# Performance work log

Hardware: AMD Instinct MI355X
Metric: run time of the kernel (lower is better)

## Reference

```python
import jax, jax.numpy as jnp
import numpy as np

N, M, K, C = 2048, 2048, 32, 256
AW, NE, H, S = 32, 128, 8, 32
LMAX = 2
HID = min(128, AW // 2)          # 16, hidden width of radial MLPs
EC = AW + NE + C                 # 416, edge feature dim
M0 = 2 * AW * (LMAX + 1)         # 192, q/k degree-dot feature dim
SLICES = [(0, 1), (1, 4), (4, 9)]  # m-slices for l = 0, 1, 2


def _ln(x, g, b, eps=1e-5):
    mu = jnp.mean(x, -1, keepdims=True)
    var = jnp.mean(jnp.square(x - mu), -1, keepdims=True)
    return (x - mu) * jax.lax.rsqrt(var + eps) * g + b


def _radial(x, w1, b1, g1, be1, w2, b2, g2, be2, w3, b3):
    # EquiformerV2-style RadialFunction: Linear->LN->SiLU x2 -> Linear
    h = jax.nn.silu(_ln(x @ w1.T + b1, g1, be1))
    h = jax.nn.silu(_ln(h @ w2.T + b2, g2, be2))
    return h @ w3.T + b3


def _so3_linear(x, W, b):
    # per-degree channel mixing; bias only on l=0. x: [..., 9, Cin], W: [3, Cout, Cin]
    outs = []
    for l, (s, e) in enumerate(SLICES):
        o = jnp.einsum('...mc,dc->...md', x[..., s:e, :], W[l])
        if l == 0:
            o = o + b
        outs.append(o)
    return jnp.concatenate(outs, axis=-2)


def _sph_all(vec):
    # real spherical harmonics l=0..2 of normalized vec, integral normalization
    v = vec / (jnp.linalg.norm(vec, axis=-1, keepdims=True) + 1e-12)
    x, y, z = v[..., 0], v[..., 1], v[..., 2]
    y0 = jnp.full(x.shape, 0.28209479177387814)
    c1 = 0.4886025119029199
    c2a, c2b, c2c = 1.0925484305920792, 0.31539156525252005, 0.5462742152960396
    return jnp.stack([y0, c1 * y, c1 * z, c1 * x,
                      c2a * x * y, c2a * y * z, c2b * (3.0 * z * z - 1.0),
                      c2a * x * z, c2c * (x * x - y * y)], axis=-1)


def _smooth_leaky(x, a=0.2):
    return 0.5 * (1 + a) * x + 0.5 * (1 - a) * x * (2.0 * jax.nn.sigmoid(x) - 1.0)


def _forward(node_pos, node_irreps_input, edge_dis, edge_vec, attn_weight,
             cluster_irreps_input, tgt_emb, W_dot, b_dot,
             rm0_w1, rm0_b1, rm0_g1, rm0_be1, rm0_w2, rm0_b2, rm0_g2, rm0_be2, rm0_w3, rm0_b3,
             fc_m0_w, fc_m0_b, an_g, an_b, alpha_dot,
             rv_w1, rv_b1, rv_g1, rv_be1, rv_w2, rv_b2, rv_g2, rv_be2, rv_w3, rv_b3,
             wz, bz, atomic_numbers, attn_mask, f_sparse_idx_expnode):
    n, k = attn_weight.shape[0], attn_weight.shape[1]
    aw = jnp.where(attn_mask, 0.0, attn_weight)                 # mask padded neighbors
    tgt = tgt_emb[atomic_numbers]                               # [N,NE]
    idx = f_sparse_idx_expnode                                  # [N,K] cluster gather index
    cl_scal = cluster_irreps_input[:, 0, :][idx]                # [N,K,C] scalar (l=0) part
    x_edge = jnp.concatenate(
        [aw, jnp.broadcast_to(tgt[:, None, :], (n, k, tgt.shape[-1])), cl_scal], -1)

    # dot_alpha attention logits: per-degree <feat, Y_l(r_ij)> for query and gathered key
    q = _so3_linear(node_irreps_input, W_dot, b_dot)            # [N,9,AW]
    key = _so3_linear(cluster_irreps_input, W_dot, b_dot)[idx]  # [N,K,9,AW]
    sh = _sph_all(edge_vec)                                     # [N,K,9]
    dots = [jnp.einsum('nmc,nkm->nkc', q[:, s:e, :], sh[..., s:e]) for s, e in SLICES]
    dots += [jnp.einsum('nkmc,nkm->nkc', key[:, :, s:e, :], sh[..., s:e]) for s, e in SLICES]
    m0 = jnp.concatenate(dots, -1)                              # [N,K,M0]

    ew = _radial(x_edge, rm0_w1, rm0_b1, rm0_g1, rm0_be1, rm0_w2, rm0_b2, rm0_g2, rm0_be2, rm0_w3, rm0_b3)
    af = ((m0 * ew) @ fc_m0_w.T + fc_m0_b).reshape(n, k, H, S)
    af = _smooth_leaky(_ln(af, an_g, an_b))
    logits = jnp.einsum('nkhs,hs->nkh', af, alpha_dot)
    logits = jnp.where(attn_mask, -1e9, logits)
    alpha = jax.nn.softmax(logits, axis=1)                      # [N,K,H]

    # zero-order value path: radial edge weight modulates gathered equivariant values
    vw = _radial(x_edge, rv_w1, rv_b1, rv_g1, rv_be1, rv_w2, rv_b2, rv_g2, rv_be2, rv_w3, rv_b3)
    v = (cluster_irreps_input[idx] * vw[:, :, None, :]).reshape(n, k, 9, H, C // H)
    out = jnp.einsum('nkh,nkmhc->nmhc', alpha, v).reshape(n, 9, C)
    return _so3_linear(out, wz, bz)                             # [N,9,C]


def setup_inputs() -> dict:
    ks = iter(jax.random.split(jax.random.key(0), 64))
    nrm = lambda shape, s=1.0: jax.random.normal(next(ks), shape, jnp.float32) * s
    inp = {}
    inp['node_pos'] = nrm((N, 3))
    inp['node_irreps_input'] = nrm((N, 9, C))
    inp['edge_dis'] = jax.random.uniform(next(ks), (N, K), jnp.float32) * 5.0
    inp['edge_vec'] = nrm((N, K, 3))
    inp['attn_weight'] = nrm((N, K, AW))
    inp['atomic_numbers'] = jax.random.randint(next(ks), (N,), 0, 256)
    inp['attn_mask'] = jax.random.bernoulli(next(ks), 0.1, (N, K, 1))
    inp['f_sparse_idx_expnode'] = jax.random.randint(next(ks), (N, K), 0, M)
    inp['cluster_irreps_input'] = nrm((M, 9, C))
    inp['tgt_emb'] = jax.random.uniform(next(ks), (256, NE), jnp.float32, -0.001, 0.001)
    inp['W_dot'] = nrm((3, AW, C), C ** -0.5)
    inp['b_dot'] = jnp.zeros((AW,), jnp.float32)

    def rad_params(pfx, out_dim):
        d = {}
        d[pfx + '_w1'] = nrm((HID, EC), EC ** -0.5); d[pfx + '_b1'] = jnp.zeros((HID,), jnp.float32)
        d[pfx + '_g1'] = jnp.ones((HID,), jnp.float32); d[pfx + '_be1'] = jnp.zeros((HID,), jnp.float32)
        d[pfx + '_w2'] = nrm((HID, HID), HID ** -0.5); d[pfx + '_b2'] = jnp.zeros((HID,), jnp.float32)
        d[pfx + '_g2'] = jnp.ones((HID,), jnp.float32); d[pfx + '_be2'] = jnp.zeros((HID,), jnp.float32)
        d[pfx + '_w3'] = nrm((out_dim, HID), HID ** -0.5); d[pfx + '_b3'] = jnp.zeros((out_dim,), jnp.float32)
        return d

    inp.update(rad_params('rm0', M0))
    inp['fc_m0_w'] = nrm((H * S, M0), M0 ** -0.5)
    inp['fc_m0_b'] = jnp.zeros((H * S,), jnp.float32)
    inp['an_g'] = jnp.ones((S,), jnp.float32)
    inp['an_b'] = jnp.zeros((S,), jnp.float32)
    std = S ** -0.5
    inp['alpha_dot'] = jax.random.uniform(next(ks), (H, S), jnp.float32, -std, std)
    inp.update(rad_params('rv', C))
    inp['wz'] = nrm((3, C, C), C ** -0.5)
    inp['bz'] = jnp.zeros((C,), jnp.float32)
    return inp


def reference(node_pos, node_irreps_input, edge_dis, edge_vec, attn_weight, atomic_numbers,
              attn_mask, f_sparse_idx_expnode, cluster_irreps_input, tgt_emb, W_dot, b_dot,
              rm0_w1, rm0_b1, rm0_g1, rm0_be1, rm0_w2, rm0_b2, rm0_g2, rm0_be2, rm0_w3, rm0_b3,
              fc_m0_w, fc_m0_b, an_g, an_b, alpha_dot,
              rv_w1, rv_b1, rv_g1, rv_be1, rv_w2, rv_b2, rv_g2, rv_be2, rv_w3, rv_b3,
              wz, bz):
    return _forward(node_pos, node_irreps_input, edge_dis, edge_vec, attn_weight,
                    cluster_irreps_input, tgt_emb, W_dot, b_dot,
                    rm0_w1, rm0_b1, rm0_g1, rm0_be1, rm0_w2, rm0_b2, rm0_g2, rm0_be2, rm0_w3, rm0_b3,
                    fc_m0_w, fc_m0_b, an_g, an_b, alpha_dot,
                    rv_w1, rv_b1, rv_g1, rv_be1, rv_w2, rv_b2, rv_g2, rv_be2, rv_w3, rv_b3,
                    wz, bz, atomic_numbers, attn_mask, f_sparse_idx_expnode)
```

## Files before the change

kernel.cpp:

```cpp
#include <hip/hip_runtime.h>
#include <math.h>

#define NNODE 2048
#define MCLUS 2048
#define KNBR  32
#define CDIM  256
#define HHEAD 8

typedef __attribute__((ext_vector_type(8))) short bf16x8;
typedef __attribute__((ext_vector_type(4))) float f32x4;

__device__ __forceinline__ float sigf(float x) { return 1.0f / (1.0f + __expf(-x)); }

__device__ __forceinline__ unsigned short f2bf(float f) {
    unsigned x = __float_as_uint(f);
    unsigned r = ((x >> 16) & 1u) + 0x7FFFu;
    return (unsigned short)((x + r) >> 16);
}
__device__ __forceinline__ float bf2f(unsigned short u) {
    return __uint_as_float(((unsigned)u) << 16);
}

__device__ __forceinline__ bool edge_masked(const void* mp, int mode, int e) {
    if (mode & 2) return ((const float*)mp)[e] != 0.0f;
    if (mode & 1) return ((const unsigned char*)mp)[e] != 0;
    return ((const int*)mp)[e] != 0;
}

__global__ __launch_bounds__(256) void kprep(
    const unsigned int* __restrict__ mw, int* __restrict__ flag,
    const float* __restrict__ clus, const float* __restrict__ fcw,
    const float* __restrict__ wz,
    unsigned short* __restrict__ clh, unsigned short* __restrict__ fcwh,
    unsigned short* __restrict__ wzh,
    const float* __restrict__ tgt_emb,
    const float* __restrict__ rm0_w1, const float* __restrict__ rv_w1,
    float* __restrict__ TA, float* __restrict__ CA,
    const float* __restrict__ nodei, const float* __restrict__ W_dot,
    const float* __restrict__ b_dot,
    float* __restrict__ q_ws, unsigned short* __restrict__ keyh)
{
    __shared__ __align__(16) unsigned short Xb[32][264];
    __shared__ __align__(16) unsigned short Wb[32][264];
    __shared__ int rx[32], rmm[32];
    int b = blockIdx.x, t = threadIdx.x;

    if (b < 1152) {
        int l, vr0, nm, moff;
        if (b < 128)      { l = 0; vr0 = b * 32;         nm = 1; moff = 0; }
        else if (b < 512) { l = 1; vr0 = (b - 128) * 32; nm = 3; moff = 1; }
        else              { l = 2; vr0 = (b - 512) * 32; nm = 5; moff = 4; }
        if (t < 32) {
            int vr = vr0 + t;
            rx[t] = vr / nm;
            rmm[t] = moff + vr % nm;
        }
        __syncthreads();
        for (int e = t; e < 32 * 256; e += 256) {
            int r = e >> 8, c = e & 255;
            int x = rx[r], m = rmm[r];
            const float* src = (x < NNODE) ? (nodei + ((size_t)x * 9 + m) * 256)
                                           : (clus + ((size_t)(x - NNODE) * 9 + m) * 256);
            Xb[r][c] = f2bf(src[c]);
            Wb[r][c] = f2bf(W_dot[((size_t)l * 32 + r) * 256 + c]);
        }
        __syncthreads();

        int wid = t >> 6, lane = t & 63;
        int lrow = lane & 15, kgrp = lane >> 4;
        int mt = wid >> 1, nt = wid & 1;
        f32x4 acc = (f32x4){0.f, 0.f, 0.f, 0.f};
#pragma unroll
        for (int kk = 0; kk < 8; ++kk) {
            bf16x8 a8 = *(const bf16x8*)&Xb[mt * 16 + lrow][kk * 32 + kgrp * 8];
            bf16x8 b8 = *(const bf16x8*)&Wb[nt * 16 + lrow][kk * 32 + kgrp * 8];
            acc = __builtin_amdgcn_mfma_f32_16x16x32_bf16(a8, b8, acc, 0, 0, 0);
        }
        int dcol = nt * 16 + lrow;
        float bias = (l == 0) ? b_dot[dcol] : 0.0f;
#pragma unroll
        for (int r = 0; r < 4; ++r) {
            int row = mt * 16 + kgrp * 4 + r;
            int x = rx[row], m = rmm[row];
            float val = acc[r] + bias;
            if (x < NNODE) q_ws[((size_t)x * 9 + m) * 32 + dcol] = val;
            else           keyh[((size_t)(x - NNODE) * 9 + m) * 32 + dcol] = f2bf(val);
        }
    } else if (b < 4160) {
        int bb = b - 1152;
        if (bb < MCLUS) {
            size_t base = (size_t)bb * 2304;
#pragma unroll
            for (int r = 0; r < 9; ++r) {
                int o = r * 256 + t;
                clh[base + o] = f2bf(clus[base + o]);
            }
        } else if (bb < MCLUS + 192) {
            int off = (bb - MCLUS) * 256 + t;
            fcwh[off] = f2bf(fcw[off]);
        } else {
            int off = (bb - MCLUS - 192) * 256 + t;
            wzh[off] = f2bf(wz[off]);
        }
    } else if (b < 4448) {
        int bb = b - 4160;
        int slot = t & 31, j = slot & 15, mlp = slot >> 4;
        const float* w1 = mlp ? rv_w1 : rm0_w1;
        if (bb < 32) {
            int a = bb * 8 + (t >> 5);
            const float* x = tgt_emb + (size_t)a * 128;
            const float* w = w1 + j * 416 + 32;
            float acc = 0.0f;
            for (int i = 0; i < 128; i += 4)
                acc = fmaf(x[i], w[i], fmaf(x[i+1], w[i+1], fmaf(x[i+2], w[i+2], fmaf(x[i+3], w[i+3], acc))));
            TA[a * 32 + slot] = acc;
        } else {
            int m = (bb - 32) * 8 + (t >> 5);
            const float* x = clus + (size_t)m * 2304;
            const float* w = w1 + j * 416 + 160;
            float acc = 0.0f;
            for (int i = 0; i < 256; i += 4)
                acc = fmaf(x[i], w[i], fmaf(x[i+1], w[i+1], fmaf(x[i+2], w[i+2], fmaf(x[i+3], w[i+3], acc))));
            CA[m * 32 + slot] = acc;
        }
    } else {
        int i = (b - 4448) * 256 + t;
        unsigned int w = mw[i];
        int vb = (w != 0u && w != 1u && w != 0x3F800000u) ? 1 : 0;
        int vf = (w == 0x3F800000u) ? 1 : 0;
        unsigned long long bal_b = __ballot(vb);
        unsigned long long bal_f = __ballot(vf);
        if ((t & 63) == 0) {
            if (bal_b) atomicOr(flag, 1);
            if (bal_f) atomicOr(flag, 2);
        }
    }
}

__device__ __forceinline__ float lnsilu16(float x, float g, float b) {
    float s = x;
#pragma unroll
    for (int m = 1; m < 16; m <<= 1) s += __shfl_xor(s, m, 16);
    float mu = s * 0.0625f;
    float d = x - mu;
    float s2 = d * d;
#pragma unroll
    for (int m = 1; m < 16; m <<= 1) s2 += __shfl_xor(s2, m, 16);
    float y = d * rsqrtf(s2 * 0.0625f + 1e-5f) * g + b;
    return y * sigf(y);
}

__global__ __launch_bounds__(256, 2) void k2abc(
    const float* __restrict__ attn_weight, const void* __restrict__ mask,
    const int* __restrict__ mflag,
    const int* __restrict__ f_idx, const float* __restrict__ edge_vec,
    const int* __restrict__ atom_num, const unsigned short* __restrict__ clh,
    const float* __restrict__ q_ws, const unsigned short* __restrict__ keyh,
    const float* __restrict__ TA, const float* __restrict__ CA,
    const float* __restrict__ rm0_w1, const float* __restrict__ rm0_b1,
    const float* __restrict__ rm0_g1, const float* __restrict__ rm0_be1,
    const float* __restrict__ rm0_w2, const float* __restrict__ rm0_b2,
    const float* __restrict__ rm0_g2, const float* __restrict__ rm0_be2,
    const float* __restrict__ rm0_w3, const float* __restrict__ rm0_b3,
    const unsigned short* __restrict__ fcwh, const float* __restrict__ fcb,
    const float* __restrict__ an_g, const float* __restrict__ an_b,
    const float* __restrict__ alpha_dot,
    const float* __restrict__ rv_w1, const float* __restrict__ rv_b1,
    const float* __restrict__ rv_g1, const float* __restrict__ rv_be1,
    const float* __restrict__ rv_w2, const float* __restrict__ rv_b2,
    const float* __restrict__ rv_g2, const float* __restrict__ rv_be2,
    const float* __restrict__ rv_w3, const float* __restrict__ rv_b3,
    float* __restrict__ outpre)
{
    __shared__ float qn[288];
    __shared__ float Ts[32];
    __shared__ float shS[32][9];
    __shared__ __align__(16) unsigned char poolS[32 * 200 * 2];
    float (*awS)[32] = (float(*)[32])poolS;
    float (*caS)[32] = (float(*)[32])(poolS + 4096);
    unsigned short (*mwbS)[200] = (unsigned short(*)[200])poolS;
    __shared__ unsigned short KDSh[32][96];
    __shared__ float h2mS[32][17];
    __shared__ float h2vS[32][17];
    __shared__ float lgS[32][8];
    __shared__ float alS[256];
    __shared__ float mxS[8], invS[8];
    __shared__ int idxk[32], maskk[32];

    int n = blockIdx.x, t = threadIdx.x;
    int mode = mflag[0];

    for (int i = t; i < 288; i += 256) qn[i] = q_ws[(size_t)n * 288 + i];
    if (t < 32) {
        int an = atom_num[n];
        Ts[t] = TA[an * 32 + t];
        int e = n * KNBR + t;
        idxk[t] = f_idx[e];
        maskk[t] = edge_masked(mask, mode, e) ? 1 : 0;
        float vx = edge_vec[(size_t)e * 3 + 0];
        float vy = edge_vec[(size_t)e * 3 + 1];
        float vz = edge_vec[(size_t)e * 3 + 2];
        float inv = 1.0f / (sqrtf(vx * vx + vy * vy + vz * vz) + 1e-12f);
        float x = vx * inv, y = vy * inv, z = vz * inv;
        shS[t][0] = 0.28209479177387814f;
        shS[t][1] = 0.4886025119029199f * y;
        shS[t][2] = 0.4886025119029199f * z;
        shS[t][3] = 0.4886025119029199f * x;
        shS[t][4] = 1.0925484305920792f * x * y;
        shS[t][5] = 1.0925484305920792f * y * z;
        shS[t][6] = 0.31539156525252005f * (3.0f * z * z - 1.0f);
        shS[t][7] = 1.0925484305920792f * x * z;
        shS[t][8] = 0.5462742152960396f * (x * x - y * y);
    }
    __syncthreads();
    for (int e2 = t; e2 < 1024; e2 += 256) {
        int ek = e2 >> 5, i = e2 & 31;
        awS[ek][i] = maskk[ek] ? 0.0f : attn_weight[((size_t)(n * KNBR + ek)) * 32 + i];
        caS[ek][i] = CA[(size_t)idxk[ek] * 32 + i];
    }
    for (int i = t; i < 32 * 96; i += 256) {
        int e = i / 96, j = i - e * 96;
        int p = j >> 5, c = j & 31;
        const unsigned short* kr = keyh + (size_t)idxk[e] * 288;
        float v;
        if (p == 0)      v = bf2f(kr[c]) * shS[e][0];
        else if (p == 1) v = bf2f(kr[32 + c]) * shS[e][1] + bf2f(kr[64 + c]) * shS[e][2]
                           + bf2f(kr[96 + c]) * shS[e][3];
        else             v = bf2f(kr[128 + c]) * shS[e][4] + bf2f(kr[160 + c]) * shS[e][5]
                           + bf2f(kr[192 + c]) * shS[e][6] + bf2f(kr[224 + c]) * shS[e][7]
                           + bf2f(kr[256 + c]) * shS[e][8];
        KDSh[e][j] = f2bf(v);
    }
    __syncthreads();

    {
        int g = t >> 4, j = t & 15;
        for (int ee = 0; ee < 2; ++ee) {
            int e = g + ee * 16;
            float accm = rm0_b1[j] + Ts[j] + caS[e][j];
            float accv = rv_b1[j] + Ts[16 + j] + caS[e][16 + j];
            const float* w1m = rm0_w1 + j * 416;
            const float* w1v = rv_w1 + j * 416;
#pragma unroll
            for (int i = 0; i < 32; i += 4) {
                float a0 = awS[e][i], a1 = awS[e][i + 1], a2 = awS[e][i + 2], a3 = awS[e][i + 3];
                accm = fmaf(a0, w1m[i], fmaf(a1, w1m[i+1], fmaf(a2, w1m[i+2], fmaf(a3, w1m[i+3], accm))));
                accv = fmaf(a0, w1v[i], fmaf(a1, w1v[i+1], fmaf(a2, w1v[i+2], fmaf(a3, w1v[i+3], accv))));
            }
            float hm = lnsilu16(accm, rm0_g1[j], rm0_be1[j]);
            float hv = lnsilu16(accv, rv_g1[j], rv_be1[j]);
            float am2 = rm0_b2[j], av2 = rv_b2[j];
#pragma unroll
            for (int i = 0; i < 16; ++i) {
                am2 = fmaf(__shfl(hm, i, 16), rm0_w2[j * 16 + i], am2);
                av2 = fmaf(__shfl(hv, i, 16), rv_w2[j * 16 + i], av2);
            }
            float h2m = lnsilu16(am2, rm0_g2[j], rm0_be2[j]);
            float h2v = lnsilu16(av2, rv_g2[j], rv_be2[j]);
            h2vS[e][j] = h2v;
            h2mS[e][j] = h2m;
        }
    }
    __syncthreads();

#pragma unroll
    for (int bb = 0; bb < 6; ++bb) {
#pragma unroll
        for (int r2 = 0; r2 < 4; ++r2) {
            int oi = r2 * 256 + t;
            int e = oi >> 5, c = oi & 31;
            int d = bb * 32 + c;
            const float4* w3 = (const float4*)(rm0_w3 + d * 16);
            float ew = rm0_b3[d];
#pragma unroll
            for (int i4 = 0; i4 < 4; ++i4) {
                float4 w = w3[i4];
                ew = fmaf(h2mS[e][i4 * 4 + 0], w.x, fmaf(h2mS[e][i4 * 4 + 1], w.y,
                     fmaf(h2mS[e][i4 * 4 + 2], w.z, fmaf(h2mS[e][i4 * 4 + 3], w.w, ew))));
            }
            float m0v;
            if (bb == 0)      m0v = qn[c] * shS[e][0];
            else if (bb == 1) m0v = qn[32 + c] * shS[e][1] + qn[64 + c] * shS[e][2]
                                  + qn[96 + c] * shS[e][3];
            else if (bb == 2) m0v = qn[128 + c] * shS[e][4] + qn[160 + c] * shS[e][5]
                                  + qn[192 + c] * shS[e][6] + qn[224 + c] * shS[e][7]
                                  + qn[256 + c] * shS[e][8];
            else              m0v = bf2f(KDSh[e][(bb - 3) * 32 + c]);
            mwbS[e][d] = f2bf(ew * m0v);
        }
    }
    __syncthreads();

    {
        int wid = t >> 6, lane = t & 63;
        int lrow = lane & 15, kgrp = lane >> 4;
        f32x4 acc[4][2];
#pragma unroll
        for (int i = 0; i < 4; ++i)
#pragma unroll
            for (int m = 0; m < 2; ++m) acc[i][m] = (f32x4){0.f, 0.f, 0.f, 0.f};

#pragma unroll
        for (int ntl = 0; ntl < 4; ++ntl) {
            int col = wid * 64 + ntl * 16 + lrow;
            const bf16x8* brow = (const bf16x8*)(fcwh + (size_t)col * 192);
            bf16x8 bf[6];
#pragma unroll
            for (int kk = 0; kk < 6; ++kk) bf[kk] = brow[kk * 4 + kgrp];
#pragma unroll
            for (int kk = 0; kk < 6; ++kk) {
#pragma unroll
                for (int m = 0; m < 2; ++m) {
                    bf16x8 a8 = *(const bf16x8*)&mwbS[m * 16 + lrow][kk * 32 + kgrp * 8];
                    acc[ntl][m] = __builtin_amdgcn_mfma_f32_16x16x32_bf16(a8, bf[kk], acc[ntl][m], 0, 0, 0);
                }
            }
        }
#pragma unroll
        for (int ntl = 0; ntl < 4; ++ntl) {
            float fb = fcb[wid * 64 + ntl * 16 + lrow];
#pragma unroll
            for (int m = 0; m < 2; ++m)
#pragma unroll
                for (int r = 0; r < 4; ++r) acc[ntl][m][r] += fb;
        }
        float ang0 = an_g[lrow], ang1 = an_g[16 + lrow];
        float anb0 = an_b[lrow], anb1 = an_b[16 + lrow];
#pragma unroll
        for (int hh = 0; hh < 2; ++hh) {
            int h = wid * 2 + hh;
            float ad0 = alpha_dot[h * 32 + lrow], ad1 = alpha_dot[h * 32 + 16 + lrow];
#pragma unroll
            for (int m = 0; m < 2; ++m) {
#pragma unroll
                for (int r = 0; r < 4; ++r) {
                    float a = acc[2 * hh][m][r], b = acc[2 * hh + 1][m][r];
                    float su = a + b;
#pragma unroll
                    for (int mm = 1; mm < 16; mm <<= 1) su += __shfl_xor(su, mm, 16);
                    float mu = su * (1.0f / 32.0f);
                    float da = a - mu, db = b - mu;
                    float v2 = da * da + db * db;
#pragma unroll
                    for (int mm = 1; mm < 16; mm <<= 1) v2 += __shfl_xor(v2, mm, 16);
                    float rs = rsqrtf(v2 * (1.0f / 32.0f) + 1e-5f);
                    float y0 = da * rs * ang0 + anb0;
                    float y1 = db * rs * ang1 + anb1;
                    float sl0 = 0.6f * y0 + 0.4f * y0 * (2.0f * sigf(y0) - 1.0f);
                    float sl1 = 0.6f * y1 + 0.4f * y1 * (2.0f * sigf(y1) - 1.0f);
                    float lg = sl0 * ad0 + sl1 * ad1;
#pragma unroll
                    for (int mm = 1; mm < 16; mm <<= 1) lg += __shfl_xor(lg, mm, 16);
                    if (lrow == 0) {
                        int e = m * 16 + kgrp * 4 + r;
                        lgS[e][h] = maskk[e] ? -1e9f : lg;
                    }
                }
            }
        }
    }
    __syncthreads();

    if (t < 8) {
        float mx = -1e30f;
#pragma unroll
        for (int k = 0; k < 32; ++k) mx = fmaxf(mx, lgS[k][t]);
        float sum = 0.0f;
#pragma unroll
        for (int k = 0; k < 32; ++k) sum += __expf(lgS[k][t] - mx);
        mxS[t] = mx;
        invS[t] = 1.0f / sum;
    }
    __syncthreads();
    {
        int k = t >> 3, h = t & 7;
        alS[t] = __expf(lgS[k][h] - mxS[h]) * invS[h];
    }
    __syncthreads();

    {
        int c = t, h = c >> 5;
        float w3r[16];
        const float4* w3p = (const float4*)(rv_w3 + c * 16);
#pragma unroll
        for (int i4 = 0; i4 < 4; ++i4) {
            float4 w = w3p[i4];
            w3r[i4 * 4 + 0] = w.x; w3r[i4 * 4 + 1] = w.y;
            w3r[i4 * 4 + 2] = w.z; w3r[i4 * 4 + 3] = w.w;
        }
        float b3c = rv_b3[c];
        float acc[9];
#pragma unroll
        for (int m = 0; m < 9; ++m) acc[m] = 0.0f;
        for (int k = 0; k < 32; ++k) {
            float vw = b3c;
#pragma unroll
            for (int i = 0; i < 16; ++i) vw = fmaf(h2vS[k][i], w3r[i], vw);
            float av = alS[k * 8 + h] * vw;
            const unsigned short* crow = clh + (size_t)idxk[k] * 2304 + c;
#pragma unroll
            for (int m = 0; m < 9; ++m) acc[m] = fmaf(av, bf2f(crow[m * 256]), acc[m]);
        }
#pragma unroll
        for (int m = 0; m < 9; ++m) outpre[((size_t)n * 9 + m) * 256 + c] = acc[m];
    }
}

__global__ __launch_bounds__(256) void k5_final(
    const unsigned short* __restrict__ wzh, const float* __restrict__ bz,
    float* __restrict__ io)
{
    __shared__ __align__(16) unsigned short Xb[32][264];
    __shared__ int rr[32];
    int b = blockIdx.x, t = threadIdx.x;
    int l, vr0, nm, moff;
    if (b < 64)       { l = 0; vr0 = b * 32;         nm = 1; moff = 0; }
    else if (b < 256) { l = 1; vr0 = (b - 64) * 32;  nm = 3; moff = 1; }
    else              { l = 2; vr0 = (b - 256) * 32; nm = 5; moff = 4; }
    if (t < 32) {
        int vr = vr0 + t;
        int n = vr / nm, m = moff + vr % nm;
        rr[t] = n * 9 + m;
    }
    __syncthreads();
    for (int e = t; e < 32 * 256; e += 256) {
        int r = e >> 8, c = e & 255;
        Xb[r][c] = f2bf(io[(size_t)rr[r] * 256 + c]);
    }
    __syncthreads();

    int wid = t >> 6, lane = t & 63;
    int lrow = lane & 15, kgrp = lane >> 4;
    f32x4 acc[2][4];
#pragma unroll
    for (int mt = 0; mt < 2; ++mt)
#pragma unroll
        for (int ntl = 0; ntl < 4; ++ntl) acc[mt][ntl] = (f32x4){0.f, 0.f, 0.f, 0.f};

#pragma unroll
    for (int ntl = 0; ntl < 4; ++ntl) {
        int dcol = wid * 64 + ntl * 16 + lrow;
        const bf16x8* brow = (const bf16x8*)(wzh + ((size_t)l * 256 + dcol) * 256);
#pragma unroll
        for (int kk = 0; kk < 8; ++kk) {
            bf16x8 b8 = brow[kk * 4 + kgrp];
#pragma unroll
            for (int mt = 0; mt < 2; ++mt) {
                bf16x8 a8 = *(const bf16x8*)&Xb[mt * 16 + lrow][kk * 32 + kgrp * 8];
                acc[mt][ntl] = __builtin_amdgcn_mfma_f32_16x16x32_bf16(a8, b8, acc[mt][ntl], 0, 0, 0);
            }
        }
    }
#pragma unroll
    for (int ntl = 0; ntl < 4; ++ntl) {
        int dcol = wid * 64 + ntl * 16 + lrow;
        float bias = (l == 0) ? bz[dcol] : 0.0f;
#pragma unroll
        for (int mt = 0; mt < 2; ++mt) {
#pragma unroll
            for (int r = 0; r < 4; ++r) {
                int row = mt * 16 + kgrp * 4 + r;
                io[(size_t)rr[row] * 256 + dcol] = acc[mt][ntl][r] + bias;
            }
        }
    }
}

extern "C" void kernel_launch(void* const* d_in, const int* in_sizes, int n_in,
                              void* d_out, int out_size, void* d_ws, size_t ws_size,
                              hipStream_t stream)
{
    (void)in_sizes; (void)n_in; (void)out_size; (void)ws_size;

    const float* node_irreps = (const float*)d_in[1];
    const float* edge_vec    = (const float*)d_in[3];
    const float* attn_weight = (const float*)d_in[4];
    const int*   atom_num    = (const int*)d_in[5];
    const void*  attn_mask   = d_in[6];
    const int*   f_idx       = (const int*)d_in[7];
    const float* clus        = (const float*)d_in[8];
    const float* tgt_emb     = (const float*)d_in[9];
    const float* W_dot       = (const float*)d_in[10];
    const float* b_dot       = (const float*)d_in[11];
    const float* rm0_w1 = (const float*)d_in[12];
    const float* rm0_b1 = (const float*)d_in[13];
    const float* rm0_g1 = (const float*)d_in[14];
    const float* rm0_be1 = (const float*)d_in[15];
    const float* rm0_w2 = (const float*)d_in[16];
    const float* rm0_b2 = (const float*)d_in[17];
    const float* rm0_g2 = (const float*)d_in[18];
    const float* rm0_be2 = (const float*)d_in[19];
    const float* rm0_w3 = (const float*)d_in[20];
    const float* rm0_b3 = (const float*)d_in[21];
    const float* fcw = (const float*)d_in[22];
    const float* fcb = (const float*)d_in[23];
    const float* an_g = (const float*)d_in[24];
    const float* an_b = (const float*)d_in[25];
    const float* alpha_dot = (const float*)d_in[26];
    const float* rv_w1 = (const float*)d_in[27];
    const float* rv_b1 = (const float*)d_in[28];
    const float* rv_g1 = (const float*)d_in[29];
    const float* rv_be1 = (const float*)d_in[30];
    const float* rv_w2 = (const float*)d_in[31];
    const float* rv_b2 = (const float*)d_in[32];
    const float* rv_g2 = (const float*)d_in[33];
    const float* rv_be2 = (const float*)d_in[34];
    const float* rv_w3 = (const float*)d_in[35];
    const float* rv_b3 = (const float*)d_in[36];
    const float* wz = (const float*)d_in[37];
    const float* bz = (const float*)d_in[38];

    float* ws = (float*)d_ws;
    int* flag = (int*)d_ws;
    float* q_ws = ws + 16;
    unsigned short* keyh = (unsigned short*)(q_ws + (size_t)NNODE * 288);
    float* TA_ws = (float*)(keyh + (size_t)MCLUS * 288);
    float* CA_ws = TA_ws + 256 * 32;
    unsigned short* clh = (unsigned short*)(CA_ws + (size_t)MCLUS * 32);
    unsigned short* fcwh = (unsigned short*)(clh + (size_t)MCLUS * 2304);
    unsigned short* wzh = fcwh + 256 * 192;
    float* outpre = (float*)d_out;

    hipMemsetAsync(flag, 0, sizeof(int), stream);
    kprep<<<4512, 256, 0, stream>>>(
        (const unsigned int*)attn_mask, flag,
        clus, fcw, wz, clh, fcwh, wzh,
        tgt_emb, rm0_w1, rv_w1, TA_ws, CA_ws,
        node_irreps, W_dot, b_dot, q_ws, keyh);
    k2abc<<<NNODE, 256, 0, stream>>>(
        attn_weight, attn_mask, flag, f_idx, edge_vec, atom_num, clh,
        q_ws, keyh, TA_ws, CA_ws,
        rm0_w1, rm0_b1, rm0_g1, rm0_be1, rm0_w2, rm0_b2, rm0_g2, rm0_be2, rm0_w3, rm0_b3,
        fcwh, fcb, an_g, an_b, alpha_dot,
        rv_w1, rv_b1, rv_g1, rv_be1, rv_w2, rv_b2, rv_g2, rv_be2, rv_w3, rv_b3,
        outpre);
    k5_final<<<576, 256, 0, stream>>>(wzh, bz, outpre);
}
```

Measured before the change: 198.7 us.

## Fuse final SO3 linear into attention kernel and skip masked edges

Folds the separate final per-degree linear (k5_final) into the end of the per-node attention kernel. Each block now writes its 9x256 pre-activation to shared memory as bf16, zero-pads it to 16 rows, and runs MFMA against all three degree weight matrices, writing only the rows that belong to each degree. This removes a launch and the global write/read round trip of the intermediate, but spends about 3x the MFMA work per node on padded or unused rows. It also skips masked edges in the value accumulation loop and overlays several shared arrays to limit LDS growth.

```diff
diff --git a/kernel.cpp b/kernel.cpp
--- a/kernel.cpp
+++ b/kernel.cpp
@@ -150,7 +150,7 @@
     return y * sigf(y);
 }
 
-__global__ __launch_bounds__(256, 2) void k2abc(
+__global__ __launch_bounds__(256, 2) void k2full(
     const float* __restrict__ attn_weight, const void* __restrict__ mask,
     const int* __restrict__ mflag,
     const int* __restrict__ f_idx, const float* __restrict__ edge_vec,
@@ -170,7 +170,8 @@
     const float* __restrict__ rv_w2, const float* __restrict__ rv_b2,
     const float* __restrict__ rv_g2, const float* __restrict__ rv_be2,
     const float* __restrict__ rv_w3, const float* __restrict__ rv_b3,
-    float* __restrict__ outpre)
+    const unsigned short* __restrict__ wzh, const float* __restrict__ bz,
+    float* __restrict__ outfin)
 {
     __shared__ float qn[288];
     __shared__ float Ts[32];
@@ -179,12 +180,15 @@
     float (*awS)[32] = (float(*)[32])poolS;
     float (*caS)[32] = (float(*)[32])(poolS + 4096);
     unsigned short (*mwbS)[200] = (unsigned short(*)[200])poolS;
-    __shared__ unsigned short KDSh[32][96];
+    unsigned short (*XbD)[264] = (unsigned short(*)[264])poolS;
+    __shared__ __align__(16) unsigned char pool2[6144];
+    unsigned short (*KDSh)[96] = (unsigned short(*)[96])pool2;
+    float (*lgS)[8] = (float(*)[8])pool2;
+    float* alS = (float*)(pool2 + 1024);
+    float* mxS = (float*)(pool2 + 2048);
+    float* invS = (float*)(pool2 + 2080);
     __shared__ float h2mS[32][17];
     __shared__ float h2vS[32][17];
-    __shared__ float lgS[32][8];
-    __shared__ float alS[256];
-    __shared__ float mxS[8], invS[8];
     __shared__ int idxk[32], maskk[32];
 
     int n = blockIdx.x, t = threadIdx.x;
@@ -393,6 +397,7 @@
 #pragma unroll
         for (int m = 0; m < 9; ++m) acc[m] = 0.0f;
         for (int k = 0; k < 32; ++k) {
+            if (maskk[k]) continue;
             float vw = b3c;
 #pragma unroll
             for (int i = 0; i < 16; ++i) vw = fmaf(h2vS[k][i], w3r[i], vw);
@@ -401,66 +406,43 @@
 #pragma unroll
             for (int m = 0; m < 9; ++m) acc[m] = fmaf(av, bf2f(crow[m * 256]), acc[m]);
         }
-#pragma unroll
-        for (int m = 0; m < 9; ++m) outpre[((size_t)n * 9 + m) * 256 + c] = acc[m];
-    }
-}
-
-__global__ __launch_bounds__(256) void k5_final(
-    const unsigned short* __restrict__ wzh, const float* __restrict__ bz,
-    float* __restrict__ io)
-{
-    __shared__ __align__(16) unsigned short Xb[32][264];
-    __shared__ int rr[32];
-    int b = blockIdx.x, t = threadIdx.x;
-    int l, vr0, nm, moff;
-    if (b < 64)       { l = 0; vr0 = b * 32;         nm = 1; moff = 0; }
-    else if (b < 256) { l = 1; vr0 = (b - 64) * 32;  nm = 3; moff = 1; }
-    else              { l = 2; vr0 = (b - 256) * 32; nm = 5; moff = 4; }
-    if (t < 32) {
-        int vr = vr0 + t;
-        int n = vr / nm, m = moff + vr % nm;
-        rr[t] = n * 9 + m;
-    }
-    __syncthreads();
-    for (int e = t; e < 32 * 256; e += 256) {
-        int r = e >> 8, c = e & 255;
-        Xb[r][c] = f2bf(io[(size_t)rr[r] * 256 + c]);
-    }
-    __syncthreads();
-
-    int wid = t >> 6, lane = t & 63;
-    int lrow = lane & 15, kgrp = lane >> 4;
-    f32x4 acc[2][4];
-#pragma unroll
-    for (int mt = 0; mt < 2; ++mt)
-#pragma unroll
-        for (int ntl = 0; ntl < 4; ++ntl) acc[mt][ntl] = (f32x4){0.f, 0.f, 0.f, 0.f};
-
-#pragma unroll
-    for (int ntl = 0; ntl < 4; ++ntl) {
-        int dcol = wid * 64 + ntl * 16 + lrow;
-        const bf16x8* brow = (const bf16x8*)(wzh + ((size_t)l * 256 + dcol) * 256);
-#pragma unroll
-        for (int kk = 0; kk < 8; ++kk) {
-            bf16x8 b8 = brow[kk * 4 + kgrp];
-#pragma unroll
-            for (int mt = 0; mt < 2; ++mt) {
-                bf16x8 a8 = *(const bf16x8*)&Xb[mt * 16 + lrow][kk * 32 + kgrp * 8];
-                acc[mt][ntl] = __builtin_amdgcn_mfma_f32_16x16x32_bf16(a8, b8, acc[mt][ntl], 0, 0, 0);
-            }
-        }
-    }
-#pragma unroll
-    for (int ntl = 0; ntl < 4; ++ntl) {
-        int dcol = wid * 64 + ntl * 16 + lrow;
-        float bias = (l == 0) ? bz[dcol] : 0.0f;
-#pragma unroll
-        for (int mt = 0; mt < 2; ++mt) {
-#pragma unroll
-            for (int r = 0; r < 4; ++r) {
-                int row = mt * 16 + kgrp * 4 + r;
-                io[(size_t)rr[row] * 256 + dcol] = acc[mt][ntl][r] + bias;
+        __syncthreads();
+#pragma unroll
+        for (int m = 0; m < 9; ++m) XbD[m][c] = f2bf(acc[m]);
+        for (int i = t; i < 7 * 256; i += 256) XbD[9 + (i >> 8)][i & 255] = 0;
+    }
+    __syncthreads();
+
+    {
+        int wid = t >> 6, lane = t & 63;
+        int lrow = lane & 15, kgrp = lane >> 4;
+        bf16x8 a8v[8];
+#pragma unroll
+        for (int kk = 0; kk < 8; ++kk)
+            a8v[kk] = *(const bf16x8*)&XbD[lrow][kk * 32 + kgrp * 8];
+#pragma unroll
+        for (int l = 0; l < 3; ++l) {
+#pragma unroll
+            for (int ntl = 0; ntl < 4; ++ntl) {
+                int dcol = wid * 64 + ntl * 16 + lrow;
+                const bf16x8* brow = (const bf16x8*)(wzh + ((size_t)l * 256 + dcol) * 256);
+                f32x4 acc = (f32x4){0.f, 0.f, 0.f, 0.f};
+#pragma unroll
+                for (int kk = 0; kk < 8; ++kk) {
+                    bf16x8 b8 = brow[kk * 4 + kgrp];
+                    acc = __builtin_amdgcn_mfma_f32_16x16x32_bf16(a8v[kk], b8, acc, 0, 0, 0);
+                }
+#pragma unroll
+                for (int r = 0; r < 4; ++r) {
+                    int m = kgrp * 4 + r;
+                    bool valid = (l == 0) ? (m == 0)
+                               : (l == 1) ? (m >= 1 && m <= 3)
+                                          : (m >= 4 && m <= 8);
+                    if (valid) {
+                        float v = acc[r] + ((l == 0) ? bz[dcol] : 0.0f);
+                        outfin[((size_t)n * 9 + m) * 256 + dcol] = v;
+                    }
+                }
             }
         }
     }
@@ -519,7 +501,7 @@
     unsigned short* clh = (unsigned short*)(CA_ws + (size_t)MCLUS * 32);
     unsigned short* fcwh = (unsigned short*)(clh + (size_t)MCLUS * 2304);
     unsigned short* wzh = fcwh + 256 * 192;
-    float* outpre = (float*)d_out;
+    float* outfin = (float*)d_out;
 
     hipMemsetAsync(flag, 0, sizeof(int), stream);
     kprep<<<4512, 256, 0, stream>>>(
@@ -527,12 +509,11 @@
         clus, fcw, wz, clh, fcwh, wzh,
         tgt_emb, rm0_w1, rv_w1, TA_ws, CA_ws,
         node_irreps, W_dot, b_dot, q_ws, keyh);
-    k2abc<<<NNODE, 256, 0, stream>>>(
+    k2full<<<NNODE, 256, 0, stream>>>(
         attn_weight, attn_mask, flag, f_idx, edge_vec, atom_num, clh,
         q_ws, keyh, TA_ws, CA_ws,
         rm0_w1, rm0_b1, rm0_g1, rm0_be1, rm0_w2, rm0_b2, rm0_g2, rm0_be2, rm0_w3, rm0_b3,
         fcwh, fcb, an_g, an_b, alpha_dot,
         rv_w1, rv_b1, rv_g1, rv_be1, rv_w2, rv_b2, rv_g2, rv_be2, rv_w3, rv_b3,
-        outpre);
-    k5_final<<<576, 256, 0, stream>>>(wzh, bz, outpre);
-}
+        wzh, bz, outfin);
+}
```

Result: slower. 247.9 us (+24.7%).
